# Kernel tuning notes

Measured on AMD Instinct MI355X. Metric: run time of the kernel, lower is better.

The kernel has to match this reference:

```python
import jax, jax.numpy as jnp
import numpy as np

B, S, D, H = 4, 1024, 1024, 16
E = D // H  # head_dim = 64
N = 2 * H  # number of slots


def _ln(x, g, b, eps=1e-5):
    m = x.mean(-1, keepdims=True)
    v = ((x - m) ** 2).mean(-1, keepdims=True)
    return (x - m) / jnp.sqrt(v + eps) * g + b


def _feat(x):
    # F.elu(x, 1.0) + 1.0
    return jax.nn.elu(x) + 1.0


def setup_inputs() -> dict:
    key = jax.random.key(0)
    ks = jax.random.split(key, 40)
    w = lambda k, shape: jax.random.normal(k, shape, jnp.float32) * 0.02
    z = lambda shape: jnp.zeros(shape, jnp.float32)
    o = lambda shape: jnp.ones(shape, jnp.float32)
    return {
        'x': jax.random.normal(ks[0], (B, S, D), jnp.float32),
        'ln1_g': o(D), 'ln1_b': z(D), 'ln2_g': o(D), 'ln2_b': z(D),
        'Wq': w(ks[1], (D, D)), 'bq': z(D),
        'Wk': w(ks[2], (D, D)), 'bk': z(D),
        'Wv': w(ks[3], (D, D)), 'bv': z(D),
        'Wf': w(ks[4], (D, D)), 'bf': z(D),
        'Wr1': w(ks[5], (D, 2 * D)), 'br1': z(2 * D),
        'Wr2': w(ks[6], (2 * D, D)), 'br2': z(D),
        'Wip': w(ks[7], (D, N * E)), 'bip': z(N * E),
        'Wtq': w(ks[8], (E, E)), 'btq': z(E),
        'Wtk': w(ks[9], (E, E)), 'btk': z(E),
        'Wtv': w(ks[10], (E, E)), 'btv': z(E),
        'lnp_g': o(E), 'lnp_b': z(E),
        'Wl1': w(ks[11], (E, 2 * E)), 'bl1': z(2 * E),
        'Wl2': w(ks[12], (2 * E, E)), 'bl2': z(E),
        'Wsp': w(ks[13], (2 * E, E)), 'bsp': z(E),
    }


def reference(x, ln1_g, ln1_b, ln2_g, ln2_b, Wq, bq, Wk, bk, Wv, bv, Wf, bf,
              Wr1, br1, Wr2, br2, Wip, bip, Wtq, btq, Wtk, btk, Wtv, btv,
              lnp_g, lnp_b, Wl1, bl1, Wl2, bl2, Wsp, bsp):
    xn = _ln(x, ln1_g, ln1_b)
    # main q/k/v
    q = (xn @ Wq + bq).reshape(B, S, H, E).transpose(0, 2, 1, 3) / np.sqrt(E)  # [B,H,S,E]
    k = (xn @ Wk + bk).reshape(B, S, H, E)
    v = (xn @ Wv + bv).reshape(B, S, H, E)
    kv0 = jnp.concatenate([k, v], axis=2)  # [B,S,2H,E] initial slots

    # --- competitive (slot) attention, 3 iterations ---
    inp = (xn @ Wip + bip).reshape(B, S, N, E)
    kk = _feat(inp @ Wtk + btk)          # [B,S,N,E]
    vv = inp @ Wtv + btv                 # [B,S,N,E]
    slots = kv0
    scale = 1.0 / E                      # slot_size = head_dim
    for _ in range(3):
        qq = (slots @ Wtq + btq) + kv0
        qq = _feat(qq * (E ** -0.5))
        logits = jnp.einsum('bswe,bsne->bswn', kk, qq)
        attn = jax.nn.softmax(logits, axis=3) + 1e-6
        attn = attn / attn.sum(axis=2, keepdims=True)
        upd = jnp.einsum('bswn,bswe->bsne', attn, vv)
        h = _ln(upd, lnp_g, lnp_b)
        h = jax.nn.relu(h @ Wl1 + bl1) @ Wl2 + bl2
        slots = slots + h * scale
    # slot_dropout is eval-mode identity
    slots = jnp.concatenate([kv0, slots], axis=-1) @ Wsp + bsp  # [B,S,2H,E]

    k2 = slots[:, :, :H].transpose(0, 2, 3, 1)  # [B,H,E,S]
    v2 = slots[:, :, H:].transpose(0, 2, 1, 3)  # [B,H,S,E]
    qf = _feat(q)
    kf = _feat(k2)
    score = qf @ kf                              # [B,H,S,S]
    score = score / (score.sum(-1, keepdims=True) + 1e-5)
    out = (score @ v2).transpose(0, 2, 1, 3).reshape(B, S, D)
    out = out @ Wf + bf
    out = x + out
    res = out
    h = _ln(out, ln2_g, ln2_b)
    h = jax.nn.relu(h @ Wr1 + br1) @ Wr2 + br2  # dropouts are eval-mode identity
    return res + h
```

## Files before the change

### kernel.cpp

```cpp
#include <hip/hip_runtime.h>
#include <hip/hip_bf16.h>

typedef __hip_bfloat16 bf16t;
typedef short short8 __attribute__((ext_vector_type(8)));
typedef float f32x4 __attribute__((ext_vector_type(4)));


__device__ __forceinline__ float featf(float x) { return x > 0.f ? x + 1.f : expf(x); }
__device__ __forceinline__ float ldf(const bf16t* p, size_t i) { return __bfloat162float(p[i]); }
__device__ __forceinline__ float ldf(const float* p, size_t i) { return p[i]; }
__device__ __forceinline__ void stf(bf16t* p, size_t i, float v) { p[i] = __float2bfloat16(v); }
__device__ __forceinline__ void stf(float* p, size_t i, float v) { p[i] = v; }
__device__ __forceinline__ float b2f(unsigned short u) {
    unsigned int x = ((unsigned int)u) << 16; float f; __builtin_memcpy(&f, &x, 4); return f;
}
__device__ __forceinline__ unsigned short f2b(float f) {
    bf16t h = __float2bfloat16(f); unsigned short u; __builtin_memcpy(&u, &h, 2); return u;
}
__device__ __forceinline__ void gl_lds16(const short* g, short* l) {
    __builtin_amdgcn_global_load_lds((const __attribute__((address_space(1))) unsigned int*)g,
                                     (__attribute__((address_space(3))) unsigned int*)l, 16, 0, 0);
}
#define MFMA16(a, b, c) __builtin_amdgcn_mfma_f32_16x16x32_bf16((a), (b), (c), 0, 0, 0)

__global__ __launch_bounds__(256) void fill_k(float* __restrict__ out, int n, float v) {
    int i = blockIdx.x * 256 + threadIdx.x;
    if (i < n) out[i] = v;
}

__global__ __launch_bounds__(256) void transpose_k(const float* __restrict__ W,
                                                   bf16t* __restrict__ Wt,
                                                   int R, int C) {
    __shared__ bf16t tile[32][33];
    int c0 = blockIdx.x * 32, r0 = blockIdx.y * 32;
    int tx = threadIdx.x, ty = threadIdx.y;
    #pragma unroll
    for (int i = 0; i < 32; i += 8) {
        int r = r0 + ty + i, c = c0 + tx;
        if (r < R && c < C) tile[ty + i][tx] = __float2bfloat16(W[(size_t)r * C + c]);
    }
    __syncthreads();
    #pragma unroll
    for (int i = 0; i < 32; i += 8) {
        int r = c0 + ty + i, c = r0 + tx;
        if (r < C && c < R) Wt[(size_t)r * R + c] = tile[tx][ty + i];
    }
}

__global__ __launch_bounds__(256) void small_prep_k(const float* __restrict__ Wtk,
                                                    const float* __restrict__ Wtv,
                                                    const float* __restrict__ Wtq,
                                                    const float* __restrict__ Wl1,
                                                    const float* __restrict__ Wl2,
                                                    const float* __restrict__ Wsp,
                                                    const float* __restrict__ bk,
                                                    const float* __restrict__ bv,
                                                    const float* __restrict__ bip,
                                                    const float* __restrict__ bq,
                                                    bf16t* __restrict__ WtkT,
                                                    bf16t* __restrict__ WtvT,
                                                    bf16t* __restrict__ WtqI,
                                                    bf16t* __restrict__ Wl1T,
                                                    bf16t* __restrict__ Wl2T,
                                                    bf16t* __restrict__ WspT,
                                                    float* __restrict__ bcat) {
    int b = blockIdx.x, tid = threadIdx.x;
    if (b == 0) {
        for (int i = tid; i < 4096; i += 256) { int c = i >> 6, r = i & 63; WtkT[i] = __float2bfloat16(Wtk[r * 64 + c]); }
    } else if (b == 1) {
        for (int i = tid; i < 4096; i += 256) { int c = i >> 6, r = i & 63; WtvT[i] = __float2bfloat16(Wtv[r * 64 + c]); }
    } else if (b == 2) {
        for (int i = tid; i < 8192; i += 256) {
            int e = i >> 7, k = i & 127;
            float v = (k < 64) ? Wtq[k * 64 + e] : ((k - 64 == e) ? 1.f : 0.f);
            WtqI[i] = __float2bfloat16(v);
        }
    } else if (b == 3) {
        for (int i = tid; i < 8192; i += 256) { int n = i >> 6, k = i & 63; Wl1T[i] = __float2bfloat16(Wl1[k * 128 + n]); }
    } else if (b == 4) {
        for (int i = tid; i < 8192; i += 256) { int n = i >> 7, k = i & 127; Wl2T[i] = __float2bfloat16(Wl2[k * 64 + n]); }
    } else if (b == 5) {
        for (int i = tid; i < 8192; i += 256) { int n = i >> 7, k = i & 127; WspT[i] = __float2bfloat16(Wsp[k * 64 + n]); }
    } else {
        for (int i = tid; i < 5120; i += 256) {
            float v;
            if (i < 1024) v = bk[i];
            else if (i < 2048) v = bv[i - 1024];
            else if (i < 4096) v = bip[i - 2048];
            else v = bq[i - 4096];
            bcat[i] = v;
        }
    }
}

__global__ __launch_bounds__(256) void ln_kernel(const float* __restrict__ X,
                                                 const float* __restrict__ g,
                                                 const float* __restrict__ b,
                                                 bf16t* __restrict__ Y) {
    int t = blockIdx.x, tid = threadIdx.x;
    size_t base = (size_t)t * 1024 + tid * 4;
    float v0 = X[base + 0], v1 = X[base + 1], v2 = X[base + 2], v3 = X[base + 3];
    float s = v0 + v1 + v2 + v3;
    float q = v0 * v0 + v1 * v1 + v2 * v2 + v3 * v3;
    __shared__ float rs[4], rq[4];
    for (int o = 32; o > 0; o >>= 1) { s += __shfl_down(s, o); q += __shfl_down(q, o); }
    int wid = tid >> 6, lane = tid & 63;
    if (lane == 0) { rs[wid] = s; rq[wid] = q; }
    __syncthreads();
    float S = rs[0] + rs[1] + rs[2] + rs[3];
    float Q = rq[0] + rq[1] + rq[2] + rq[3];
    float mean = S * (1.f / 1024.f);
    float var = Q * (1.f / 1024.f) - mean * mean;
    float rstd = rsqrtf(var + 1e-5f);
    int c = tid * 4;
    stf(Y, base + 0, (v0 - mean) * rstd * g[c + 0] + b[c + 0]);
    stf(Y, base + 1, (v1 - mean) * rstd * g[c + 1] + b[c + 1]);
    stf(Y, base + 2, (v2 - mean) * rstd * g[c + 2] + b[c + 2]);
    stf(Y, base + 3, (v3 - mean) * rstd * g[c + 3] + b[c + 3]);
}

template <int MODE, typename TC, typename TADD>
__global__ __launch_bounds__(256) void gemm128_k(const bf16t* __restrict__ A,
                                                 const bf16t* __restrict__ Bt,
                                                 const float* __restrict__ bias,
                                                 const TADD* __restrict__ add,
                                                 TC* __restrict__ C,
                                                 int M, int N, int K, int ldC) {
    __shared__ short As[128 * 32];
    __shared__ short Bs[128 * 32];
    int tid = threadIdx.x;
    int wave = tid >> 6, lane = tid & 63;
    int l16 = lane & 15, quad = lane >> 4;
    int tilesM = M >> 7;
    int tm = blockIdx.x % tilesM;
    int tn = blockIdx.x / tilesM;
    int wm = wave >> 1, wn = wave & 1;

    int lrow = lane >> 2;
    int lseg = (lane & 3) * 8;
    const short* Ag = (const short*)A + (size_t)(tm * 128 + wave * 32 + lrow) * K + lseg;
    const short* Ag2 = Ag + (size_t)16 * K;
    const short* Bg = (const short*)Bt + (size_t)(tn * 128 + wave * 32 + lrow) * K + lseg;
    const short* Bg2 = Bg + (size_t)16 * K;
    short* Asw = As + (wave * 32) * 32;
    short* Asw2 = Asw + 16 * 32;
    short* Bsw = Bs + (wave * 32) * 32;
    short* Bsw2 = Bsw + 16 * 32;

    f32x4 acc[4][4] = {};
    for (int k0 = 0; k0 < K; k0 += 32) {
        gl_lds16(Ag + k0, Asw);
        gl_lds16(Ag2 + k0, Asw2);
        gl_lds16(Bg + k0, Bsw);
        gl_lds16(Bg2 + k0, Bsw2);
        __syncthreads();
        short8 av[4], bv[4];
        #pragma unroll
        for (int i = 0; i < 4; i++)
            av[i] = *(const short8*)(As + (wm * 64 + i * 16 + l16) * 32 + quad * 8);
        #pragma unroll
        for (int j = 0; j < 4; j++)
            bv[j] = *(const short8*)(Bs + (wn * 64 + j * 16 + l16) * 32 + quad * 8);
        #pragma unroll
        for (int i = 0; i < 4; i++)
            #pragma unroll
            for (int j = 0; j < 4; j++)
                acc[i][j] = MFMA16(av[i], bv[j], acc[i][j]);
        __syncthreads();
    }

    #pragma unroll
    for (int j = 0; j < 4; j++) {
        int col = tn * 128 + wn * 64 + j * 16 + l16;
        float bcol = bias[col];
        #pragma unroll
        for (int i = 0; i < 4; i++) {
            int row0 = tm * 128 + wm * 64 + i * 16 + quad * 4;
            #pragma unroll
            for (int r = 0; r < 4; r++) {
                int row = row0 + r;
                float v = acc[i][j][r] + bcol;
                float outv;
                if constexpr (MODE == 0) outv = v;
                else if constexpr (MODE == 4) outv = fmaxf(v, 0.f);
                else if constexpr (MODE == 5) outv = v + ldf(add, (size_t)row * N + col);
                else outv = v;
                stf(C, (size_t)row * ldC + col, outv);
            }
        }
    }
}

__global__ __launch_bounds__(256) void gemm_proj_k(const bf16t* __restrict__ A,
                                                   const bf16t* __restrict__ Bt,
                                                   const float* __restrict__ bias,
                                                   bf16t* __restrict__ kv0,
                                                   bf16t* __restrict__ inp,
                                                   bf16t* __restrict__ qf) {
    __shared__ short As[128 * 32];
    __shared__ short Bs[128 * 32];
    const int K = 1024;
    int tid = threadIdx.x;
    int wave = tid >> 6, lane = tid & 63;
    int l16 = lane & 15, quad = lane >> 4;
    int tm = blockIdx.x & 31;
    int tn = blockIdx.x >> 5;
    int wm = wave >> 1, wn = wave & 1;

    int lrow = lane >> 2;
    int lseg = (lane & 3) * 8;
    const short* Ag = (const short*)A + (size_t)(tm * 128 + wave * 32 + lrow) * K + lseg;
    const short* Ag2 = Ag + (size_t)16 * K;
    const short* Bg = (const short*)Bt + (size_t)(tn * 128 + wave * 32 + lrow) * K + lseg;
    const short* Bg2 = Bg + (size_t)16 * K;
    short* Asw = As + (wave * 32) * 32;
    short* Asw2 = Asw + 16 * 32;
    short* Bsw = Bs + (wave * 32) * 32;
    short* Bsw2 = Bsw + 16 * 32;

    f32x4 acc[4][4] = {};
    for (int k0 = 0; k0 < K; k0 += 32) {
        gl_lds16(Ag + k0, Asw);
        gl_lds16(Ag2 + k0, Asw2);
        gl_lds16(Bg + k0, Bsw);
        gl_lds16(Bg2 + k0, Bsw2);
        __syncthreads();
        short8 av[4], bv[4];
        #pragma unroll
        for (int i = 0; i < 4; i++)
            av[i] = *(const short8*)(As + (wm * 64 + i * 16 + l16) * 32 + quad * 8);
        #pragma unroll
        for (int j = 0; j < 4; j++)
            bv[j] = *(const short8*)(Bs + (wn * 64 + j * 16 + l16) * 32 + quad * 8);
        #pragma unroll
        for (int i = 0; i < 4; i++)
            #pragma unroll
            for (int j = 0; j < 4; j++)
                acc[i][j] = MFMA16(av[i], bv[j], acc[i][j]);
        __syncthreads();
    }

    #pragma unroll
    for (int j = 0; j < 4; j++) {
        int col = tn * 128 + wn * 64 + j * 16 + l16;
        float bcol = bias[col];
        #pragma unroll
        for (int i = 0; i < 4; i++) {
            int row0 = tm * 128 + wm * 64 + i * 16 + quad * 4;
            #pragma unroll
            for (int r = 0; r < 4; r++) {
                int row = row0 + r;
                float v = acc[i][j][r] + bcol;
                if (tn < 16) stf(kv0, (size_t)row * 2048 + col, v);
                else if (tn < 32) stf(inp, (size_t)row * 2048 + (col - 2048), v);
                else stf(qf, (size_t)row * 1024 + (col - 4096), featf(v * 0.125f));
            }
        }
    }
}

template <int MODE, typename TC>
__global__ __launch_bounds__(256) void gemm_k(const bf16t* __restrict__ A,
                                              const bf16t* __restrict__ Bt,
                                              const float* __restrict__ bias,
                                              TC* __restrict__ C,
                                              int M, int N, int K, int ldC) {
    int wave = threadIdx.x >> 6;
    int lane = threadIdx.x & 63;
    int tilesN = N >> 6;
    int tiles = (M >> 6) * tilesN;
    int tile = blockIdx.x * 4 + wave;
    if (tile >= tiles) return;
    int tm = tile / tilesN, tn = tile - tm * tilesN;
    int l16 = lane & 15, quad = lane >> 4;

    f32x4 acc[4][4] = {};
    const short* Ab = (const short*)A + (size_t)(tm * 64 + l16) * K;
    const short* Bb = (const short*)Bt + (size_t)(tn * 64 + l16) * K;

    for (int k0 = 0; k0 < K; k0 += 32) {
        int ka = k0 + quad * 8;
        short8 av[4], bv[4];
        #pragma unroll
        for (int i = 0; i < 4; i++) av[i] = *(const short8*)(Ab + (size_t)i * 16 * K + ka);
        #pragma unroll
        for (int j = 0; j < 4; j++) bv[j] = *(const short8*)(Bb + (size_t)j * 16 * K + ka);
        #pragma unroll
        for (int i = 0; i < 4; i++)
            #pragma unroll
            for (int j = 0; j < 4; j++)
                acc[i][j] = MFMA16(av[i], bv[j], acc[i][j]);
    }

    #pragma unroll
    for (int j = 0; j < 4; j++) {
        int col = tn * 64 + j * 16 + l16;
        float bcol = bias[col];
        #pragma unroll
        for (int i = 0; i < 4; i++) {
            int row0 = tm * 64 + i * 16 + quad * 4;
            #pragma unroll
            for (int r = 0; r < 4; r++) {
                int row = row0 + r;
                float v = acc[i][j][r] + bcol;
                if constexpr (MODE == 7) {
                    stf(C, (size_t)(row >> 5) * 2048 + (size_t)col * 32 + (row & 31), v);
                } else {
                    float outv;
                    if constexpr (MODE == 0) outv = v;
                    else if constexpr (MODE == 1) outv = featf(v);
                    else outv = v;
                    stf(C, (size_t)row * ldC + col, outv);
                }
            }
        }
    }
}

__global__ __launch_bounds__(256) void gemm_cat_k(const bf16t* __restrict__ A1,
                                                  const bf16t* __restrict__ A2,
                                                  const bf16t* __restrict__ Bt,
                                                  const float* __restrict__ bias,
                                                  bf16t* __restrict__ C, int M) {
    int wave = threadIdx.x >> 6;
    int lane = threadIdx.x & 63;
    int tiles = M >> 6;
    int tile = blockIdx.x * 4 + wave;
    if (tile >= tiles) return;
    int tm = tile;
    int l16 = lane & 15, quad = lane >> 4;
    f32x4 acc[4][4] = {};
    #pragma unroll
    for (int p = 0; p < 2; p++) {
        const short* Ab = (const short*)(p ? A2 : A1) + (size_t)(tm * 64 + l16) * 64;
        const short* Bb = (const short*)Bt + (size_t)l16 * 128 + p * 64;
        #pragma unroll
        for (int k0 = 0; k0 < 64; k0 += 32) {
            int ka = k0 + quad * 8;
            short8 av[4], bv[4];
            #pragma unroll
            for (int i = 0; i < 4; i++) av[i] = *(const short8*)(Ab + (size_t)i * 16 * 64 + ka);
            #pragma unroll
            for (int j = 0; j < 4; j++) bv[j] = *(const short8*)(Bb + (size_t)j * 16 * 128 + ka);
            #pragma unroll
            for (int i = 0; i < 4; i++)
                #pragma unroll
                for (int j = 0; j < 4; j++)
                    acc[i][j] = MFMA16(av[i], bv[j], acc[i][j]);
        }
    }
    #pragma unroll
    for (int j = 0; j < 4; j++) {
        int col = j * 16 + l16;
        float bcol = bias[col];
        #pragma unroll
        for (int i = 0; i < 4; i++) {
            int row0 = tm * 64 + i * 16 + quad * 4;
            #pragma unroll
            for (int r = 0; r < 4; r++)
                C[(size_t)(row0 + r) * 64 + col] = __float2bfloat16(acc[i][j][r] + bcol);
        }
    }
}

__global__ __launch_bounds__(256) void slot_all_k(const bf16t* __restrict__ kv0,
                                                  const bf16t* __restrict__ kk,
                                                  const bf16t* __restrict__ vvT,
                                                  const bf16t* __restrict__ WtqI,
                                                  const float* __restrict__ btq,
                                                  const float* __restrict__ lnpg,
                                                  const float* __restrict__ lnpb,
                                                  const bf16t* __restrict__ Wl1T,
                                                  const float* __restrict__ bl1,
                                                  const bf16t* __restrict__ Wl2T,
                                                  const float* __restrict__ bl2,
                                                  bf16t* __restrict__ slots_out) {
    __shared__ short slotsS[4][32 * 72];
    __shared__ short scratch[4][32 * 72];
    int wave = threadIdx.x >> 6, lane = threadIdx.x & 63;
    int l16 = lane & 15, quad = lane >> 4;
    int t = blockIdx.x * 4 + wave;
    short* S = slotsS[wave];
    short* X = scratch[wave];
    size_t tbase = (size_t)t * 2048;

    {
        const short* src = (const short*)kv0 + tbase;
        #pragma unroll
        for (int p = 0; p < 4; p++) {
            int idx = p * 512 + lane * 8;
            int row = idx >> 6, col = idx & 63;
            *(short8*)(S + row * 72 + col) = *(const short8*)(src + idx);
        }
    }
    short8 kkf[2][2], kvf[2][2];
    #pragma unroll
    for (int i = 0; i < 2; i++)
        #pragma unroll
        for (int k0 = 0; k0 < 2; k0++) {
            size_t fo = tbase + (size_t)(i * 16 + l16) * 64 + k0 * 32 + quad * 8;
            kkf[i][k0] = *(const short8*)((const short*)kk + fo);
            kvf[i][k0] = *(const short8*)((const short*)kv0 + fo);
        }

    float btqv[4], bl2v[4], lgv[4], lbv[4], bl1v[8];
    #pragma unroll
    for (int j = 0; j < 4; j++) {
        btqv[j] = btq[j * 16 + l16]; bl2v[j] = bl2[j * 16 + l16];
        lgv[j] = lnpg[j * 16 + l16]; lbv[j] = lnpb[j * 16 + l16];
    }
    #pragma unroll
    for (int j = 0; j < 8; j++) bl1v[j] = bl1[j * 16 + l16];

    for (int it = 0; it < 3; it++) {
        f32x4 aq[2][4] = {};
        #pragma unroll
        for (int k0 = 0; k0 < 4; k0++) {
            short8 af[2];
            #pragma unroll
            for (int i = 0; i < 2; i++)
                af[i] = (k0 < 2) ? *(const short8*)(S + (i * 16 + l16) * 72 + k0 * 32 + quad * 8)
                                 : kvf[i][k0 - 2];
            #pragma unroll
            for (int j = 0; j < 4; j++) {
                short8 bf_ = *(const short8*)((const short*)WtqI + (size_t)(j * 16 + l16) * 128 + k0 * 32 + quad * 8);
                #pragma unroll
                for (int i = 0; i < 2; i++) aq[i][j] = MFMA16(af[i], bf_, aq[i][j]);
            }
        }
        #pragma unroll
        for (int i = 0; i < 2; i++)
            #pragma unroll
            for (int j = 0; j < 4; j++)
                #pragma unroll
                for (int r = 0; r < 4; r++) {
                    int n = i * 16 + quad * 4 + r, e = j * 16 + l16;
                    X[n * 72 + e] = (short)f2b(featf((aq[i][j][r] + btqv[j]) * 0.125f));
                }
        f32x4 al[2][2] = {};
        #pragma unroll
        for (int k0 = 0; k0 < 2; k0++) {
            short8 bf_[2];
            #pragma unroll
            for (int j = 0; j < 2; j++)
                bf_[j] = *(const short8*)(X + (j * 16 + l16) * 72 + k0 * 32 + quad * 8);
            #pragma unroll
            for (int i = 0; i < 2; i++)
                #pragma unroll
                for (int j = 0; j < 2; j++)
                    al[i][j] = MFMA16(kkf[i][k0], bf_[j], al[i][j]);
        }
        #pragma unroll
        for (int i = 0; i < 2; i++)
            #pragma unroll
            for (int r = 0; r < 4; r++) {
                float m = fmaxf(al[i][0][r], al[i][1][r]);
                #pragma unroll
                for (int d = 1; d < 16; d <<= 1) m = fmaxf(m, __shfl_xor(m, d));
                float e0 = expf(al[i][0][r] - m), e1 = expf(al[i][1][r] - m);
                float s = e0 + e1;
                #pragma unroll
                for (int d = 1; d < 16; d <<= 1) s += __shfl_xor(s, d);
                float inv = 1.f / s;
                al[i][0][r] = e0 * inv + 1e-6f;
                al[i][1][r] = e1 * inv + 1e-6f;
            }
        #pragma unroll
        for (int j = 0; j < 2; j++) {
            float cs = 0.f;
            #pragma unroll
            for (int i = 0; i < 2; i++)
                #pragma unroll
                for (int r = 0; r < 4; r++) cs += al[i][j][r];
            cs += __shfl_xor(cs, 16);
            cs += __shfl_xor(cs, 32);
            float inv = 1.f / cs;
            #pragma unroll
            for (int i = 0; i < 2; i++)
                #pragma unroll
                for (int r = 0; r < 4; r++) al[i][j][r] *= inv;
        }
        #pragma unroll
        for (int i = 0; i < 2; i++)
            #pragma unroll
            for (int j = 0; j < 2; j++)
                #pragma unroll
                for (int r = 0; r < 4; r++) {
                    int w = i * 16 + quad * 4 + r, n = j * 16 + l16;
                    X[n * 40 + w] = (short)f2b(al[i][j][r]);
                }
        f32x4 au[2][4] = {};
        {
            short8 af[2];
            #pragma unroll
            for (int i = 0; i < 2; i++)
                af[i] = *(const short8*)(X + (i * 16 + l16) * 40 + quad * 8);
            #pragma unroll
            for (int j = 0; j < 4; j++) {
                short8 bf_ = *(const short8*)((const short*)vvT + tbase + (size_t)(j * 16 + l16) * 32 + quad * 8);
                #pragma unroll
                for (int i = 0; i < 2; i++) au[i][j] = MFMA16(af[i], bf_, au[i][j]);
            }
        }
        #pragma unroll
        for (int i = 0; i < 2; i++)
            #pragma unroll
            for (int r = 0; r < 4; r++) {
                float s1 = 0.f, s2 = 0.f;
                #pragma unroll
                for (int j = 0; j < 4; j++) { float u = au[i][j][r]; s1 += u; s2 += u * u; }
                #pragma unroll
                for (int d = 1; d < 16; d <<= 1) { s1 += __shfl_xor(s1, d); s2 += __shfl_xor(s2, d); }
                float mean = s1 * (1.f / 64.f);
                float var = s2 * (1.f / 64.f) - mean * mean;
                float rstd = rsqrtf(var + 1e-5f);
                int n = i * 16 + quad * 4 + r;
                #pragma unroll
                for (int j = 0; j < 4; j++)
                    X[n * 72 + j * 16 + l16] = (short)f2b((au[i][j][r] - mean) * rstd * lgv[j] + lbv[j]);
            }
        short8 a1[2][2];
        #pragma unroll
        for (int i = 0; i < 2; i++)
            #pragma unroll
            for (int k0 = 0; k0 < 2; k0++)
                a1[i][k0] = *(const short8*)(X + (i * 16 + l16) * 72 + k0 * 32 + quad * 8);
        f32x4 ac2[2][4] = {};
        #pragma unroll
        for (int c = 0; c < 2; c++) {
            f32x4 ac1[2][4] = {};
            #pragma unroll
            for (int k0 = 0; k0 < 2; k0++)
                #pragma unroll
                for (int j = 0; j < 4; j++) {
                    short8 bf_ = *(const short8*)((const short*)Wl1T + (size_t)((c * 4 + j) * 16 + l16) * 64 + k0 * 32 + quad * 8);
                    #pragma unroll
                    for (int i = 0; i < 2; i++) ac1[i][j] = MFMA16(a1[i][k0], bf_, ac1[i][j]);
                }
            #pragma unroll
            for (int i = 0; i < 2; i++)
                #pragma unroll
                for (int j = 0; j < 4; j++)
                    #pragma unroll
                    for (int r = 0; r < 4; r++) {
                        int n = i * 16 + quad * 4 + r;
                        X[n * 72 + j * 16 + l16] = (short)f2b(fmaxf(ac1[i][j][r] + bl1v[c * 4 + j], 0.f));
                    }
            #pragma unroll
            for (int kc = 0; kc < 2; kc++) {
                short8 a2[2];
                #pragma unroll
                for (int i = 0; i < 2; i++)
                    a2[i] = *(const short8*)(X + (i * 16 + l16) * 72 + kc * 32 + quad * 8);
                int k1 = c * 2 + kc;
                #pragma unroll
                for (int j = 0; j < 4; j++) {
                    short8 bf_ = *(const short8*)((const short*)Wl2T + (size_t)(j * 16 + l16) * 128 + k1 * 32 + quad * 8);
                    #pragma unroll
                    for (int i = 0; i < 2; i++) ac2[i][j] = MFMA16(a2[i], bf_, ac2[i][j]);
                }
            }
        }
        #pragma unroll
        for (int i = 0; i < 2; i++)
            #pragma unroll
            for (int j = 0; j < 4; j++)
                #pragma unroll
                for (int r = 0; r < 4; r++) {
                    int n = i * 16 + quad * 4 + r, e = j * 16 + l16;
                    float old = b2f((unsigned short)S[n * 72 + e]);
                    S[n * 72 + e] = (short)f2b(old + (ac2[i][j][r] + bl2v[j]) * (1.f / 64.f));
                }
    }
    {
        short* dst = (short*)slots_out + tbase;
        #pragma unroll
        for (int p = 0; p < 4; p++) {
            int idx = p * 512 + lane * 8;
            int row = idx >> 6, col = idx & 63;
            *(short8*)(dst + idx) = *(const short8*)(S + row * 72 + col);
        }
    }
}

__global__ __launch_bounds__(256) void kv_outer_k(const bf16t* __restrict__ slotsO,
                                                  float* __restrict__ Kmat,
                                                  float* __restrict__ ksum) {
    __shared__ short kfT[64 * 72];
    __shared__ short v2T[64 * 72];
    __shared__ float ksred[8][64];
    int bh = blockIdx.x;
    int b = bh >> 4, h = bh & 15;
    int tid = threadIdx.x;
    int wave = tid >> 6, lane = tid & 63;
    int l16 = lane & 15, quad = lane >> 4;
    int m0 = wave * 16;

    int sgrp = tid >> 5;
    int e0 = (tid & 31) * 2;
    float ks0 = 0.f, ks1 = 0.f;
    f32x4 acc[4];
    #pragma unroll
    for (int j = 0; j < 4; j++) acc[j] = (f32x4){0.f, 0.f, 0.f, 0.f};

    for (int tile = 0; tile < 16; tile++) {
        #pragma unroll
        for (int p = 0; p < 8; p++) {
            int sl = p * 8 + sgrp;
            size_t row = ((size_t)(b * 1024 + tile * 64 + sl)) * 2048;
            unsigned int dk = *(const unsigned int*)((const unsigned short*)slotsO + row + h * 64 + e0);
            float f0 = featf(b2f((unsigned short)(dk & 0xffff)));
            float f1 = featf(b2f((unsigned short)(dk >> 16)));
            ks0 += f0; ks1 += f1;
            kfT[e0 * 72 + sl] = (short)f2b(f0);
            kfT[(e0 + 1) * 72 + sl] = (short)f2b(f1);
            unsigned int dv = *(const unsigned int*)((const unsigned short*)slotsO + row + (16 + h) * 64 + e0);
            v2T[e0 * 72 + sl] = (short)(dv & 0xffff);
            v2T[(e0 + 1) * 72 + sl] = (short)(dv >> 16);
        }
        __syncthreads();
        #pragma unroll
        for (int k2 = 0; k2 < 2; k2++) {
            short8 a = *(const short8*)(kfT + (m0 + l16) * 72 + k2 * 32 + quad * 8);
            #pragma unroll
            for (int j = 0; j < 4; j++) {
                short8 bv = *(const short8*)(v2T + (j * 16 + l16) * 72 + k2 * 32 + quad * 8);
                acc[j] = MFMA16(a, bv, acc[j]);
            }
        }
        __syncthreads();
    }

    float* Km = Kmat + (size_t)bh * 4096;
    #pragma unroll
    for (int j = 0; j < 4; j++)
        #pragma unroll
        for (int r = 0; r < 4; r++)
            Km[(m0 + quad * 4 + r) * 64 + j * 16 + l16] = acc[j][r];

    ksred[sgrp][e0] = ks0;
    ksred[sgrp][e0 + 1] = ks1;
    __syncthreads();
    if (tid < 64) {
        float s = 0.f;
        #pragma unroll
        for (int r = 0; r < 8; r++) s += ksred[r][tid];
        ksum[bh * 64 + tid] = s;
    }
}

__global__ __launch_bounds__(256) void attn_out_k(const bf16t* __restrict__ qf,
                                                  const float* __restrict__ Kmat,
                                                  const float* __restrict__ ksum,
                                                  bf16t* __restrict__ out) {
    int t = blockIdx.x, tid = threadIdx.x;
    int b = t >> 10;
    __shared__ float q[16 * 65];
    __shared__ float dinv[16];
    for (int i = tid; i < 1024; i += 256) {
        int h = i >> 6, e = i & 63;
        q[h * 65 + e] = __bfloat162float(qf[(size_t)t * 1024 + i]);
    }
    __syncthreads();
    if (tid < 16) {
        int bh = b * 16 + tid;
        float d = 0.f;
        for (int e = 0; e < 64; e++) d += q[tid * 65 + e] * ksum[bh * 64 + e];
        dinv[tid] = 1.f / (d + 1e-5f);
    }
    __syncthreads();
    int h = tid >> 4, j0 = (tid & 15) * 4;
    const float* Km = Kmat + (size_t)(b * 16 + h) * 4096;
    float a0 = 0.f, a1 = 0.f, a2 = 0.f, a3 = 0.f;
    for (int e = 0; e < 64; e++) {
        float qe = q[h * 65 + e];
        const float* kr = Km + e * 64 + j0;
        a0 += qe * kr[0]; a1 += qe * kr[1]; a2 += qe * kr[2]; a3 += qe * kr[3];
    }
    float di = dinv[h];
    size_t ob = (size_t)t * 1024 + h * 64 + j0;
    out[ob + 0] = __float2bfloat16(a0 * di);
    out[ob + 1] = __float2bfloat16(a1 * di);
    out[ob + 2] = __float2bfloat16(a2 * di);
    out[ob + 3] = __float2bfloat16(a3 * di);
}

#define LAUNCH_GEMM(MODE, TCT, A_, Bt_, bias_, C_, M_, N_, K_, ldC_)                         \
    do {                                                                                     \
        int tiles__ = ((M_) >> 6) * ((N_) >> 6);                                             \
        gemm_k<MODE, TCT><<<(tiles__ + 3) / 4, 256, 0, stream>>>(                            \
            (const bf16t*)(A_), (const bf16t*)(Bt_), (const float*)(bias_),                  \
            (TCT*)(C_), (M_), (N_), (K_), (ldC_));                                           \
    } while (0)

#define LAUNCH_GEMM128(MODE, TCT, TADDT, A_, Bt_, bias_, add_, C_, M_, N_, K_, ldC_)         \
    do {                                                                                     \
        int tiles__ = ((M_) >> 7) * ((N_) >> 7);                                             \
        gemm128_k<MODE, TCT, TADDT><<<tiles__, 256, 0, stream>>>(                            \
            (const bf16t*)(A_), (const bf16t*)(Bt_), (const float*)(bias_),                  \
            (const TADDT*)(add_), (TCT*)(C_), (M_), (N_), (K_), (ldC_));                     \
    } while (0)

extern "C" void kernel_launch(void* const* d_in, const int* in_sizes, int n_in,
                              void* d_out, int out_size, void* d_ws, size_t ws_size,
                              hipStream_t stream) {
    (void)in_sizes; (void)n_in;
    const float* x    = (const float*)d_in[0];
    const float* ln1g = (const float*)d_in[1];
    const float* ln1b = (const float*)d_in[2];
    const float* ln2g = (const float*)d_in[3];
    const float* ln2b = (const float*)d_in[4];
    const float* Wq  = (const float*)d_in[5];  const float* bq  = (const float*)d_in[6];
    const float* Wk  = (const float*)d_in[7];  const float* bk  = (const float*)d_in[8];
    const float* Wv  = (const float*)d_in[9];  const float* bv  = (const float*)d_in[10];
    const float* Wf  = (const float*)d_in[11]; const float* bWf = (const float*)d_in[12];
    const float* Wr1 = (const float*)d_in[13]; const float* br1 = (const float*)d_in[14];
    const float* Wr2 = (const float*)d_in[15]; const float* br2 = (const float*)d_in[16];
    const float* Wip = (const float*)d_in[17]; const float* bip = (const float*)d_in[18];
    const float* Wtq = (const float*)d_in[19]; const float* btq = (const float*)d_in[20];
    const float* Wtk = (const float*)d_in[21]; const float* btk = (const float*)d_in[22];
    const float* Wtv = (const float*)d_in[23]; const float* btv = (const float*)d_in[24];
    const float* lnpg= (const float*)d_in[25]; const float* lnpb= (const float*)d_in[26];
    const float* Wl1 = (const float*)d_in[27]; const float* bl1 = (const float*)d_in[28];
    const float* Wl2 = (const float*)d_in[29]; const float* bl2 = (const float*)d_in[30];
    const float* Wsp = (const float*)d_in[31]; const float* bsp = (const float*)d_in[32];

    char* ws = (char*)d_ws;
    size_t off = 0;
    auto alloc = [&](size_t bytes) -> char* {
        off = (off + 255) & ~(size_t)255;
        char* p = ws + off;
        off += bytes;
        return p;
    };
    const size_t T = 4096, TS = 131072;
    const size_t MB8 = T * 1024 * 2, MB16 = T * 2048 * 2;
    bf16t* R_xn   = (bf16t*)alloc(MB8);
    bf16t* R_h1   = (bf16t*)alloc(MB8);
    bf16t* R_kv0  = (bf16t*)alloc(MB16);
    bf16t* R_inp  = (bf16t*)alloc(MB16);
    bf16t* R_kk   = (bf16t*)alloc(MB16);
    bf16t* R_vv   = (bf16t*)alloc(MB16);
    bf16t* R_sl   = (bf16t*)alloc(MB16);
    bf16t* Wcat   = (bf16t*)alloc(5120 * 1024 * 2);
    bf16t* WtkT = (bf16t*)alloc(64 * 64 * 2);
    bf16t* WtvT = (bf16t*)alloc(64 * 64 * 2);
    bf16t* WtqI = (bf16t*)alloc(64 * 128 * 2);
    bf16t* Wl1T = (bf16t*)alloc(128 * 64 * 2);
    bf16t* Wl2T = (bf16t*)alloc(64 * 128 * 2);
    bf16t* WspT = (bf16t*)alloc(64 * 128 * 2);
    float* bcat = (float*)alloc(5120 * 4);
    float* Kmat = (float*)alloc(64 * 4096 * 4);
    float* ksum = (float*)alloc(64 * 64 * 4);

    if (off > ws_size) {
        fill_k<<<(out_size + 255) / 256, 256, 0, stream>>>((float*)d_out, out_size, 1000.f);
        return;
    }
    float* R_res = (float*)R_vv;

    auto tr = [&](const float* W, bf16t* Wt, int R, int C) {
        dim3 g((C + 31) / 32, (R + 31) / 32), blk(32, 8);
        transpose_k<<<g, blk, 0, stream>>>(W, Wt, R, C);
    };

    small_prep_k<<<7, 256, 0, stream>>>(Wtk, Wtv, Wtq, Wl1, Wl2, Wsp, bk, bv, bip, bq,
                                        WtkT, WtvT, WtqI, Wl1T, Wl2T, WspT, bcat);

    ln_kernel<<<4096, 256, 0, stream>>>(x, ln1g, ln1b, R_xn);

    tr(Wk, Wcat, 1024, 1024);
    tr(Wv, Wcat + (size_t)1024 * 1024, 1024, 1024);
    tr(Wip, Wcat + (size_t)2048 * 1024, 1024, 2048);
    tr(Wq, Wcat + (size_t)4096 * 1024, 1024, 1024);

    gemm_proj_k<<<1280, 256, 0, stream>>>(R_xn, Wcat, bcat, R_kv0, R_inp, R_h1);

    LAUNCH_GEMM(1, bf16t, R_inp, WtkT, btk, R_kk, 131072, 64, 64, 64);
    LAUNCH_GEMM(7, bf16t, R_inp, WtvT, btv, R_vv, 131072, 64, 64, 64);

    slot_all_k<<<1024, 256, 0, stream>>>(R_kv0, R_kk, R_vv, WtqI, btq, lnpg, lnpb,
                                         Wl1T, bl1, Wl2T, bl2, R_sl);

    gemm_cat_k<<<512, 256, 0, stream>>>(R_kv0, R_sl, WspT, bsp, R_kk, 131072);

    kv_outer_k<<<64, 256, 0, stream>>>(R_kk, Kmat, ksum);

    attn_out_k<<<4096, 256, 0, stream>>>(R_h1, Kmat, ksum, R_inp);

    tr(Wf, Wcat, 1024, 1024);
    LAUNCH_GEMM128(5, float, float, R_inp, Wcat, bWf, x, R_res, 4096, 1024, 1024, 1024);

    ln_kernel<<<4096, 256, 0, stream>>>(R_res, ln2g, ln2b, R_xn);
    tr(Wr1, Wcat, 1024, 2048);
    LAUNCH_GEMM128(4, bf16t, bf16t, R_xn, Wcat, br1, nullptr, R_sl, 4096, 2048, 1024, 2048);
    tr(Wr2, Wcat, 2048, 1024);
    LAUNCH_GEMM128(5, float, float, R_sl, Wcat, br2, R_res, (float*)d_out, 4096, 1024, 2048, 1024);
}
```

Before: 617.0 us.

## Split each slot-attention token across two waves with shared LDS reductions

The slot-attention kernel now assigns each token (32 slots) to two waves that each own 16 slot rows, instead of one wave per token. The waves share the q-feature and attention matrices in LDS and combine column sums through a small shared buffer, with block barriers between phases. This halves per-wave register and LDS footprint and doubles the grid to expose more parallelism and occupancy, at the cost of three __syncthreads per iteration and cross-wave coordination.

```diff
diff --git a/kernel.cpp b/kernel.cpp
--- a/kernel.cpp
+++ b/kernel.cpp
@@ -375,33 +375,34 @@
                                                   const bf16t* __restrict__ Wl2T,
                                                   const float* __restrict__ bl2,
                                                   bf16t* __restrict__ slots_out) {
-    __shared__ short slotsS[4][32 * 72];
-    __shared__ short scratch[4][32 * 72];
+    __shared__ short slotsW[4][16 * 72];
+    __shared__ short Xt[2][32 * 72];
+    __shared__ float csum[2][2][32];
     int wave = threadIdx.x >> 6, lane = threadIdx.x & 63;
     int l16 = lane & 15, quad = lane >> 4;
-    int t = blockIdx.x * 4 + wave;
-    short* S = slotsS[wave];
-    short* X = scratch[wave];
+    int tok = wave >> 1, half = wave & 1;
+    int t = blockIdx.x * 2 + tok;
+    int r0 = half * 16;
+    short* S = slotsW[wave];
+    short* X = Xt[tok];
     size_t tbase = (size_t)t * 2048;
 
     {
-        const short* src = (const short*)kv0 + tbase;
-        #pragma unroll
-        for (int p = 0; p < 4; p++) {
+        const short* src = (const short*)kv0 + tbase + (size_t)r0 * 64;
+        #pragma unroll
+        for (int p = 0; p < 2; p++) {
             int idx = p * 512 + lane * 8;
             int row = idx >> 6, col = idx & 63;
             *(short8*)(S + row * 72 + col) = *(const short8*)(src + idx);
         }
     }
-    short8 kkf[2][2], kvf[2][2];
-    #pragma unroll
-    for (int i = 0; i < 2; i++)
-        #pragma unroll
-        for (int k0 = 0; k0 < 2; k0++) {
-            size_t fo = tbase + (size_t)(i * 16 + l16) * 64 + k0 * 32 + quad * 8;
-            kkf[i][k0] = *(const short8*)((const short*)kk + fo);
-            kvf[i][k0] = *(const short8*)((const short*)kv0 + fo);
-        }
+    short8 kkf[2], kvf[2];
+    #pragma unroll
+    for (int k0 = 0; k0 < 2; k0++) {
+        size_t fo = tbase + (size_t)(r0 + l16) * 64 + k0 * 32 + quad * 8;
+        kkf[k0] = *(const short8*)((const short*)kk + fo);
+        kvf[k0] = *(const short8*)((const short*)kv0 + fo);
+    }
 
     float btqv[4], bl2v[4], lgv[4], lbv[4], bl1v[8];
     #pragma unroll
@@ -413,169 +414,136 @@
     for (int j = 0; j < 8; j++) bl1v[j] = bl1[j * 16 + l16];
 
     for (int it = 0; it < 3; it++) {
-        f32x4 aq[2][4] = {};
-        #pragma unroll
-        for (int k0 = 0; k0 < 4; k0++) {
-            short8 af[2];
-            #pragma unroll
-            for (int i = 0; i < 2; i++)
-                af[i] = (k0 < 2) ? *(const short8*)(S + (i * 16 + l16) * 72 + k0 * 32 + quad * 8)
-                                 : kvf[i][k0 - 2];
-            #pragma unroll
-            for (int j = 0; j < 4; j++) {
-                short8 bf_ = *(const short8*)((const short*)WtqI + (size_t)(j * 16 + l16) * 128 + k0 * 32 + quad * 8);
+        {
+            f32x4 aq[4] = {};
+            #pragma unroll
+            for (int k0 = 0; k0 < 4; k0++) {
+                short8 af = (k0 < 2) ? *(const short8*)(S + l16 * 72 + k0 * 32 + quad * 8)
+                                     : kvf[k0 - 2];
                 #pragma unroll
-                for (int i = 0; i < 2; i++) aq[i][j] = MFMA16(af[i], bf_, aq[i][j]);
-            }
-        }
-        #pragma unroll
-        for (int i = 0; i < 2; i++)
+                for (int j = 0; j < 4; j++) {
+                    short8 bf_ = *(const short8*)((const short*)WtqI + (size_t)(j * 16 + l16) * 128 + k0 * 32 + quad * 8);
+                    aq[j] = MFMA16(af, bf_, aq[j]);
+                }
+            }
             #pragma unroll
             for (int j = 0; j < 4; j++)
                 #pragma unroll
                 for (int r = 0; r < 4; r++) {
-                    int n = i * 16 + quad * 4 + r, e = j * 16 + l16;
-                    X[n * 72 + e] = (short)f2b(featf((aq[i][j][r] + btqv[j]) * 0.125f));
+                    int n = r0 + quad * 4 + r, e = j * 16 + l16;
+                    X[n * 72 + e] = (short)f2b(featf((aq[j][r] + btqv[j]) * 0.125f));
                 }
-        f32x4 al[2][2] = {};
+        }
+        __syncthreads();
+        f32x4 al[2] = {};
         #pragma unroll
         for (int k0 = 0; k0 < 2; k0++) {
-            short8 bf_[2];
-            #pragma unroll
-            for (int j = 0; j < 2; j++)
-                bf_[j] = *(const short8*)(X + (j * 16 + l16) * 72 + k0 * 32 + quad * 8);
-            #pragma unroll
-            for (int i = 0; i < 2; i++)
-                #pragma unroll
-                for (int j = 0; j < 2; j++)
-                    al[i][j] = MFMA16(kkf[i][k0], bf_[j], al[i][j]);
-        }
-        #pragma unroll
-        for (int i = 0; i < 2; i++)
-            #pragma unroll
-            for (int r = 0; r < 4; r++) {
-                float m = fmaxf(al[i][0][r], al[i][1][r]);
-                #pragma unroll
-                for (int d = 1; d < 16; d <<= 1) m = fmaxf(m, __shfl_xor(m, d));
-                float e0 = expf(al[i][0][r] - m), e1 = expf(al[i][1][r] - m);
-                float s = e0 + e1;
-                #pragma unroll
-                for (int d = 1; d < 16; d <<= 1) s += __shfl_xor(s, d);
-                float inv = 1.f / s;
-                al[i][0][r] = e0 * inv + 1e-6f;
-                al[i][1][r] = e1 * inv + 1e-6f;
-            }
+            #pragma unroll
+            for (int j = 0; j < 2; j++) {
+                short8 bf_ = *(const short8*)(X + (j * 16 + l16) * 72 + k0 * 32 + quad * 8);
+                al[j] = MFMA16(kkf[k0], bf_, al[j]);
+            }
+        }
+        #pragma unroll
+        for (int r = 0; r < 4; r++) {
+            float m = fmaxf(al[0][r], al[1][r]);
+            #pragma unroll
+            for (int d = 1; d < 16; d <<= 1) m = fmaxf(m, __shfl_xor(m, d));
+            float e0 = expf(al[0][r] - m), e1 = expf(al[1][r] - m);
+            float s = e0 + e1;
+            #pragma unroll
+            for (int d = 1; d < 16; d <<= 1) s += __shfl_xor(s, d);
+            float inv = 1.f / s;
+            al[0][r] = e0 * inv + 1e-6f;
+            al[1][r] = e1 * inv + 1e-6f;
+        }
         #pragma unroll
         for (int j = 0; j < 2; j++) {
-            float cs = 0.f;
-            #pragma unroll
-            for (int i = 0; i < 2; i++)
-                #pragma unroll
-                for (int r = 0; r < 4; r++) cs += al[i][j][r];
+            float cs = al[j][0] + al[j][1] + al[j][2] + al[j][3];
             cs += __shfl_xor(cs, 16);
             cs += __shfl_xor(cs, 32);
-            float inv = 1.f / cs;
-            #pragma unroll
-            for (int i = 0; i < 2; i++)
-                #pragma unroll
-                for (int r = 0; r < 4; r++) al[i][j][r] *= inv;
-        }
-        #pragma unroll
-        for (int i = 0; i < 2; i++)
-            #pragma unroll
-            for (int j = 0; j < 2; j++)
-                #pragma unroll
-                for (int r = 0; r < 4; r++) {
-                    int w = i * 16 + quad * 4 + r, n = j * 16 + l16;
-                    X[n * 40 + w] = (short)f2b(al[i][j][r]);
-                }
-        f32x4 au[2][4] = {};
+            if (quad == 0) csum[tok][half][j * 16 + l16] = cs;
+        }
+        __syncthreads();
+        #pragma unroll
+        for (int j = 0; j < 2; j++) {
+            int n = j * 16 + l16;
+            float inv = 1.f / (csum[tok][0][n] + csum[tok][1][n]);
+            #pragma unroll
+            for (int r = 0; r < 4; r++)
+                X[n * 72 + r0 + quad * 4 + r] = (short)f2b(al[j][r] * inv);
+        }
+        __syncthreads();
+        f32x4 au[4] = {};
         {
-            short8 af[2];
-            #pragma unroll
-            for (int i = 0; i < 2; i++)
-                af[i] = *(const short8*)(X + (i * 16 + l16) * 40 + quad * 8);
+            short8 af = *(const short8*)(X + (r0 + l16) * 72 + quad * 8);
             #pragma unroll
             for (int j = 0; j < 4; j++) {
                 short8 bf_ = *(const short8*)((const short*)vvT + tbase + (size_t)(j * 16 + l16) * 32 + quad * 8);
-                #pragma unroll
-                for (int i = 0; i < 2; i++) au[i][j] = MFMA16(af[i], bf_, au[i][j]);
-            }
-        }
-        #pragma unroll
-        for (int i = 0; i < 2; i++)
-            #pragma unroll
-            for (int r = 0; r < 4; r++) {
-                float s1 = 0.f, s2 = 0.f;
-                #pragma unroll
-                for (int j = 0; j < 4; j++) { float u = au[i][j][r]; s1 += u; s2 += u * u; }
-                #pragma unroll
-                for (int d = 1; d < 16; d <<= 1) { s1 += __shfl_xor(s1, d); s2 += __shfl_xor(s2, d); }
-                float mean = s1 * (1.f / 64.f);
-                float var = s2 * (1.f / 64.f) - mean * mean;
-                float rstd = rsqrtf(var + 1e-5f);
-                int n = i * 16 + quad * 4 + r;
-                #pragma unroll
-                for (int j = 0; j < 4; j++)
-                    X[n * 72 + j * 16 + l16] = (short)f2b((au[i][j][r] - mean) * rstd * lgv[j] + lbv[j]);
-            }
-        short8 a1[2][2];
-        #pragma unroll
-        for (int i = 0; i < 2; i++)
-            #pragma unroll
-            for (int k0 = 0; k0 < 2; k0++)
-                a1[i][k0] = *(const short8*)(X + (i * 16 + l16) * 72 + k0 * 32 + quad * 8);
-        f32x4 ac2[2][4] = {};
+                au[j] = MFMA16(af, bf_, au[j]);
+            }
+        }
+        #pragma unroll
+        for (int r = 0; r < 4; r++) {
+            float s1 = 0.f, s2 = 0.f;
+            #pragma unroll
+            for (int j = 0; j < 4; j++) { float u = au[j][r]; s1 += u; s2 += u * u; }
+            #pragma unroll
+            for (int d = 1; d < 16; d <<= 1) { s1 += __shfl_xor(s1, d); s2 += __shfl_xor(s2, d); }
+            float mean = s1 * (1.f / 64.f);
+            float var = s2 * (1.f / 64.f) - mean * mean;
+            float rstd = rsqrtf(var + 1e-5f);
+            int n = r0 + quad * 4 + r;
+            #pragma unroll
+            for (int j = 0; j < 4; j++)
+                X[n * 72 + j * 16 + l16] = (short)f2b((au[j][r] - mean) * rstd * lgv[j] + lbv[j]);
+        }
+        short8 a1[2];
+        #pragma unroll
+        for (int k0 = 0; k0 < 2; k0++)
+            a1[k0] = *(const short8*)(X + (r0 + l16) * 72 + k0 * 32 + quad * 8);
+        f32x4 ac2[4] = {};
         #pragma unroll
         for (int c = 0; c < 2; c++) {
-            f32x4 ac1[2][4] = {};
+            f32x4 ac1[4] = {};
             #pragma unroll
             for (int k0 = 0; k0 < 2; k0++)
                 #pragma unroll
                 for (int j = 0; j < 4; j++) {
                     short8 bf_ = *(const short8*)((const short*)Wl1T + (size_t)((c * 4 + j) * 16 + l16) * 64 + k0 * 32 + quad * 8);
-                    #pragma unroll
-                    for (int i = 0; i < 2; i++) ac1[i][j] = MFMA16(a1[i][k0], bf_, ac1[i][j]);
+                    ac1[j] = MFMA16(a1[k0], bf_, ac1[j]);
                 }
             #pragma unroll
-            for (int i = 0; i < 2; i++)
+            for (int j = 0; j < 4; j++)
                 #pragma unroll
-                for (int j = 0; j < 4; j++)
-                    #pragma unroll
-                    for (int r = 0; r < 4; r++) {
-                        int n = i * 16 + quad * 4 + r;
-                        X[n * 72 + j * 16 + l16] = (short)f2b(fmaxf(ac1[i][j][r] + bl1v[c * 4 + j], 0.f));
-                    }
+                for (int r = 0; r < 4; r++) {
+                    int n = r0 + quad * 4 + r;
+                    X[n * 72 + j * 16 + l16] = (short)f2b(fmaxf(ac1[j][r] + bl1v[c * 4 + j], 0.f));
+                }
             #pragma unroll
             for (int kc = 0; kc < 2; kc++) {
-                short8 a2[2];
-                #pragma unroll
-                for (int i = 0; i < 2; i++)
-                    a2[i] = *(const short8*)(X + (i * 16 + l16) * 72 + kc * 32 + quad * 8);
+                short8 a2 = *(const short8*)(X + (r0 + l16) * 72 + kc * 32 + quad * 8);
                 int k1 = c * 2 + kc;
                 #pragma unroll
                 for (int j = 0; j < 4; j++) {
                     short8 bf_ = *(const short8*)((const short*)Wl2T + (size_t)(j * 16 + l16) * 128 + k1 * 32 + quad * 8);
-                    #pragma unroll
-                    for (int i = 0; i < 2; i++) ac2[i][j] = MFMA16(a2[i], bf_, ac2[i][j]);
+                    ac2[j] = MFMA16(a2, bf_, ac2[j]);
                 }
             }
         }
         #pragma unroll
-        for (int i = 0; i < 2; i++)
-            #pragma unroll
-            for (int j = 0; j < 4; j++)
-                #pragma unroll
-                for (int r = 0; r < 4; r++) {
-                    int n = i * 16 + quad * 4 + r, e = j * 16 + l16;
-                    float old = b2f((unsigned short)S[n * 72 + e]);
-                    S[n * 72 + e] = (short)f2b(old + (ac2[i][j][r] + bl2v[j]) * (1.f / 64.f));
-                }
+        for (int j = 0; j < 4; j++)
+            #pragma unroll
+            for (int r = 0; r < 4; r++) {
+                int nl = quad * 4 + r, e = j * 16 + l16;
+                float old = b2f((unsigned short)S[nl * 72 + e]);
+                S[nl * 72 + e] = (short)f2b(old + (ac2[j][r] + bl2v[j]) * (1.f / 64.f));
+            }
     }
     {
-        short* dst = (short*)slots_out + tbase;
-        #pragma unroll
-        for (int p = 0; p < 4; p++) {
+        short* dst = (short*)slots_out + tbase + (size_t)r0 * 64;
+        #pragma unroll
+        for (int p = 0; p < 2; p++) {
             int idx = p * 512 + lane * 8;
             int row = idx >> 6, col = idx & 63;
             *(short8*)(dst + idx) = *(const short8*)(S + row * 72 + col);
@@ -779,7 +747,7 @@
     LAUNCH_GEMM(1, bf16t, R_inp, WtkT, btk, R_kk, 131072, 64, 64, 64);
     LAUNCH_GEMM(7, bf16t, R_inp, WtvT, btv, R_vv, 131072, 64, 64, 64);
 
-    slot_all_k<<<1024, 256, 0, stream>>>(R_kv0, R_kk, R_vv, WtqI, btq, lnpg, lnpb,
+    slot_all_k<<<2048, 256, 0, stream>>>(R_kv0, R_kk, R_vv, WtqI, btq, lnpg, lnpb,
                                          Wl1T, bl1, Wl2T, bl2, R_sl);
 
     gemm_cat_k<<<512, 256, 0, stream>>>(R_kv0, R_sl, WspT, bsp, R_kk, 131072);
```

New measurement: 652.2 us. 5.7% more time.
